# Optimization experiments

Hardware: AMD Instinct MI355X
Metric: run time of the kernel (lower is better)

## Reference

```python
import jax, jax.numpy as jnp
import numpy as np

B, S, DM, DE, H, DH, DC, DCq, DR = 4, 2048, 1024, 1024, 16, 64, 128, 128, 32
SCALE = 1.0 / np.sqrt(DH + DR)


def _rope_tables(seq_len, dim, theta=10000.0):
    inv = 1.0 / (theta ** (jnp.arange(0, dim, 2, dtype=jnp.float32) / dim))  # [dim/2]
    t = jnp.arange(seq_len, dtype=jnp.float32)
    ang = t[:, None] * inv[None, :]  # [S, dim/2]
    return jnp.cos(ang), jnp.sin(ang)


def _apply_rope(xq, xk, cos, sin):
    # xq, xk: [B, S, H, DR]; complex rotary on (even, odd) pairs
    def rot(x):
        s = x.shape
        xr = x.reshape(*s[:-1], s[-1] // 2, 2)
        r, i = xr[..., 0], xr[..., 1]
        c = cos[None, :s[1], None, :]
        sn = sin[None, :s[1], None, :]
        out = jnp.stack([r * c - i * sn, r * sn + i * c], axis=-1)
        return out.reshape(s)
    return rot(xq), rot(xk)


def setup_inputs() -> dict:
    key = jax.random.key(0)
    ks = jax.random.split(key, 10)
    def lin(k, din, dout):
        return 0.02 * jax.random.normal(k, (din, dout), jnp.float32)
    inp = {
        "x": jax.random.normal(ks[0], (B, S, DM), jnp.float32),
        "mask": jnp.tril(jnp.ones((S, S), jnp.float32))[None, None],
        "W_dkv": lin(ks[1], DM, DC),  "b_dkv": jnp.zeros((DC,), jnp.float32),
        "W_dq":  lin(ks[2], DM, DCq), "b_dq":  jnp.zeros((DCq,), jnp.float32),
        "W_uk":  lin(ks[3], DC, DE),  "b_uk":  jnp.zeros((DE,), jnp.float32),
        "W_uv":  lin(ks[4], DC, DE),  "b_uv":  jnp.zeros((DE,), jnp.float32),
        "W_uq":  lin(ks[5], DCq, DE), "b_uq":  jnp.zeros((DE,), jnp.float32),
        "W_qr":  lin(ks[6], DCq, DR * H), "b_qr": jnp.zeros((DR * H,), jnp.float32),
        "W_kr":  lin(ks[7], DM, DR),  "b_kr": jnp.zeros((DR,), jnp.float32),
        "W_o":   lin(ks[8], DE, DM),  "b_o":  jnp.zeros((DM,), jnp.float32),
    }
    return inp


def reference(x, mask, W_dkv, b_dkv, W_dq, b_dq, W_uk, b_uk, W_uv, b_uv,
              W_uq, b_uq, W_qr, b_qr, W_kr, b_kr, W_o, b_o):
    bs, seq_len, _ = x.shape
    cos, sin = _rope_tables(2 * S, DR)

    c_q = x @ W_dq + b_dq            # [B,S,DCq]
    c_kv = x @ W_dkv + b_dkv         # [B,S,DC]
    k_r = x @ W_kr + b_kr            # [B,S,DR]

    q_c = (c_q @ W_uq + b_uq).reshape(bs, seq_len, H, DH)
    k_c = (c_kv @ W_uk + b_uk).reshape(bs, seq_len, H, DH)
    v_c = (c_kv @ W_uv + b_uv).reshape(bs, seq_len, H, DH)

    q_r = (c_q @ W_qr + b_qr).reshape(bs, seq_len, H, DR)
    k_r = jnp.broadcast_to(k_r[:, :, None, :], (bs, seq_len, H, DR))
    q_r, k_r = _apply_rope(q_r, k_r, cos, sin)

    q_t = jnp.concatenate([q_c, q_r], axis=-1)  # [B,S,H,DH+DR]
    k_t = jnp.concatenate([k_c, k_r], axis=-1)

    attn = jnp.einsum('bqhd,bkhd->bhqk', q_t, k_t) * SCALE  # [B,H,S,S]
    m = jnp.where(mask == 0, -jnp.inf, mask)  # faithful masked_fill then add
    attn = attn + m
    p = jax.nn.softmax(attn, axis=-1)
    out = jnp.einsum('bhqk,bkhd->bqhd', p, v_c).reshape(bs, seq_len, H * DH)
    return out @ W_o + b_o
```

## Files before the change

kernel.cpp:

```cpp
#include <hip/hip_runtime.h>
#include <cstdint>
#include <cstddef>

#define S_ 2048
#define B_ 4
#define H_ 16
#define ALPHA_Q 0.14724394f

typedef __attribute__((ext_vector_type(8))) __bf16 bf16x8;
typedef __attribute__((ext_vector_type(4))) __bf16 bf16x4;
typedef __attribute__((ext_vector_type(4))) float f32x4;
typedef __attribute__((ext_vector_type(16))) float f32x16;

__device__ __forceinline__ f32x16 mfma32(bf16x8 a, bf16x8 b, f32x16 c) {
  return __builtin_amdgcn_mfma_f32_32x32x16_bf16(a, b, c, 0, 0, 0);
}

__device__ __forceinline__ void gll16(const void* g, void* l) {
  __builtin_amdgcn_global_load_lds(
      (__attribute__((address_space(1))) void*)(uintptr_t)g,
      (__attribute__((address_space(3))) void*)(uint32_t)(uintptr_t)l,
      16, 0, 0);
}

__device__ __forceinline__ int cvtpk(float lo, float hi) {
  int r;
  asm("v_cvt_pk_bf16_f32 %0, %1, %2" : "=v"(r) : "v"(lo), "v"(hi));
  return r;
}

union PAU { int w[4]; bf16x8 v; };

__device__ __forceinline__ bf16x8 packPA(int hi, float a0, float a1, float a2,
                                         float a3, float b0, float b1, float b2,
                                         float b3) {
  const int Ylo = cvtpk(a0, a1);
  const int Yhi = cvtpk(a2, a3);
  const int Xlo = cvtpk(b0, b1);
  const int Xhi = cvtpk(b2, b3);
  const int t0 = __shfl_xor(hi ? Ylo : Xlo, 32);
  const int t1 = __shfl_xor(hi ? Yhi : Xhi, 32);
  PAU u;
  u.w[0] = hi ? t0 : Ylo;
  u.w[1] = hi ? t1 : Yhi;
  u.w[2] = hi ? Xlo : t0;
  u.w[3] = hi ? Xhi : t1;
  return u.v;
}

__device__ __forceinline__ float tmax16(const f32x16& v) {
  float a[8];
#pragma unroll
  for (int i = 0; i < 8; ++i) a[i] = fmaxf(v[i], v[i + 8]);
#pragma unroll
  for (int s = 4; s > 0; s >>= 1)
#pragma unroll
    for (int i = 0; i < s; ++i) a[i] = fmaxf(a[i], a[i + s]);
  return a[0];
}

__global__ __launch_bounds__(256) void mla_prep(
    const float* __restrict__ x, __bf16* __restrict__ xb,
    const float* __restrict__ W_dq, const float* __restrict__ W_dkv,
    const float* __restrict__ W_kr, const float* __restrict__ W_uq,
    const float* __restrict__ W_qr, const float* __restrict__ W_uk,
    const float* __restrict__ W_uv, const float* __restrict__ W_o,
    __bf16* __restrict__ WdT, __bf16* __restrict__ WuqT,
    __bf16* __restrict__ WukvT, __bf16* __restrict__ WoT,
    const float* __restrict__ b_dq, const float* __restrict__ b_dkv,
    const float* __restrict__ b_kr, const float* __restrict__ b_uq,
    const float* __restrict__ b_qr, const float* __restrict__ b_uk,
    const float* __restrict__ b_uv, float* __restrict__ bias_d,
    float* __restrict__ bias_uq, float* __restrict__ bias_ukv,
    float* __restrict__ ropec, float* __restrict__ ropes) {
  const int id = blockIdx.x;
  const int t = threadIdx.x;
  __shared__ float tile[32][33];

  if (id < 4096) {
    const size_t i = ((size_t)id * 256 + t) * 8;
    float4 a = *(const float4*)&x[i];
    float4 b = *(const float4*)&x[i + 4];
    bf16x8 v;
    v[0] = (__bf16)a.x; v[1] = (__bf16)a.y; v[2] = (__bf16)a.z; v[3] = (__bf16)a.w;
    v[4] = (__bf16)b.x; v[5] = (__bf16)b.y; v[6] = (__bf16)b.z; v[7] = (__bf16)b.w;
    *(bf16x8*)&xb[i] = v;
    return;
  }
  if (id < 5856) {
    int rel = id - 4096;
    const float* W;
    __bf16* WT;
    int K, N, nt;
    if (rel < 128)      { W = W_dq;  WT = WdT;                      K = 1024; N = 128;  nt = 4; }
    else if (rel < 256) { W = W_dkv; WT = WdT + (size_t)128 * 1024; K = 1024; N = 128;  nt = 4;  rel -= 128; }
    else if (rel < 288) { W = W_kr;  WT = WdT + (size_t)256 * 1024; K = 1024; N = 32;   nt = 1;  rel -= 256; }
    else if (rel < 416) { W = W_uq;  WT = WuqT;                     K = 128;  N = 1024; nt = 32; rel -= 288; }
    else if (rel < 480) { W = W_qr;  WT = WuqT + (size_t)1024 * 128; K = 128; N = 512;  nt = 16; rel -= 416; }
    else if (rel < 608) { W = W_uk;  WT = WukvT;                    K = 128;  N = 1024; nt = 32; rel -= 480; }
    else if (rel < 736) { W = W_uv;  WT = WukvT + (size_t)1024 * 128; K = 128; N = 1024; nt = 32; rel -= 608; }
    else                { W = W_o;   WT = WoT;                      K = 1024; N = 1024; nt = 32; rel -= 736; }
    const int n0 = (rel % nt) * 32, k0 = (rel / nt) * 32;
    const int tx = t & 31, ty = t >> 5;
#pragma unroll
    for (int i = 0; i < 32; i += 8)
      tile[ty + i][tx] = W[(size_t)(k0 + ty + i) * N + n0 + tx];
    __syncthreads();
#pragma unroll
    for (int i = 0; i < 32; i += 8)
      WT[(size_t)(n0 + ty + i) * K + k0 + tx] = (__bf16)tile[tx][ty + i];
    return;
  }
  if (id < 5984) {
    const int g = (id - 5856) * 256 + t;
    const int s = g >> 4, i = g & 15;
    const float inv = exp2f(-(float)i * (13.287712379549449f / 16.0f));
    const float ang = (float)s * inv;
    ropec[g] = cosf(ang);
    ropes[g] = sinf(ang);
    return;
  }
  {
    const int g = (id - 5984) * 256 + t;
    if (g < 384)
      bias_d[g] = (g < 128) ? b_dq[g] : (g < 256) ? b_dkv[g - 128]
                 : (g < 288) ? b_kr[g - 256] : 0.f;
    if (g < 1536) bias_uq[g] = (g < 1024) ? b_uq[g] : b_qr[g - 1024];
    if (g < 2048) bias_ukv[g] = (g < 1024) ? b_uk[g] : b_uv[g - 1024];
  }
}

template <int MODE>
__global__ __launch_bounds__(256) void gemm32(
    const __bf16* __restrict__ A, int lda, const __bf16* __restrict__ BT, int ldbt,
    const float* __restrict__ bias, void* __restrict__ C0, int ldc, int K) {
  const int n0 = blockIdx.x * 128;
  const int m0 = blockIdx.y * 128;
  const int wave = threadIdx.x >> 6, lane = threadIdx.x & 63;
  const int hi = lane >> 5, lq = lane & 31;
  const int wm = (wave >> 1) * 64, wn = (wave & 1) * 64;
  __shared__ __bf16 __attribute__((aligned(16))) ldsA[8 * 128 * 8];
  __shared__ __bf16 __attribute__((aligned(16))) ldsB[8 * 128 * 8];

  const f32x16 fz16 = {0.f, 0.f, 0.f, 0.f, 0.f, 0.f, 0.f, 0.f,
                       0.f, 0.f, 0.f, 0.f, 0.f, 0.f, 0.f, 0.f};
  f32x16 acc00 = fz16, acc01 = fz16, acc10 = fz16, acc11 = fz16;

  for (int k0 = 0; k0 < K; k0 += 64) {
    __syncthreads();
#pragma unroll
    for (int i = 0; i < 8; ++i) {
      const int c = wave * 8 + i;
      if (c < 16) {
        const int sl = c >> 1, half = c & 1;
        gll16(&A[(size_t)(m0 + half * 64 + lane) * lda + k0 + sl * 8],
              &ldsA[(sl * 128 + half * 64) * 8]);
      } else {
        const int cc = c - 16;
        const int sl = cc >> 1, half = cc & 1;
        gll16(&BT[(size_t)(n0 + half * 64 + lane) * ldbt + k0 + sl * 8],
              &ldsB[(sl * 128 + half * 64) * 8]);
      }
    }
    __syncthreads();

#pragma unroll
    for (int ks = 0; ks < 4; ++ks) {
      const int sl = ks * 2 + hi;
      bf16x8 a0 = *(const bf16x8*)&ldsA[(sl * 128 + wm + lq) * 8];
      bf16x8 a1 = *(const bf16x8*)&ldsA[(sl * 128 + wm + 32 + lq) * 8];
      bf16x8 b0 = *(const bf16x8*)&ldsB[(sl * 128 + wn + lq) * 8];
      bf16x8 b1 = *(const bf16x8*)&ldsB[(sl * 128 + wn + 32 + lq) * 8];
      acc00 = mfma32(a0, b0, acc00);
      acc01 = mfma32(a0, b1, acc01);
      acc10 = mfma32(a1, b0, acc10);
      acc11 = mfma32(a1, b1, acc11);
    }
  }

  const f32x16* accs[2][2] = {{&acc00, &acc01}, {&acc10, &acc11}};
#pragma unroll
  for (int ni = 0; ni < 2; ++ni) {
    const int col = n0 + wn + ni * 32 + lq;
    const float bv = bias[col];
#pragma unroll
    for (int mi = 0; mi < 2; ++mi) {
      const f32x16& ac = *accs[mi][ni];
#pragma unroll
      for (int r = 0; r < 16; ++r) {
        const int row = m0 + wm + mi * 32 + (r & 3) + 8 * (r >> 2) + 4 * hi;
        const float v = ac[r] + bv;
        if (MODE == 0)
          ((__bf16*)C0)[(size_t)row * ldc + col] = (__bf16)v;
        else
          ((float*)C0)[(size_t)row * ldc + col] = v;
      }
    }
  }
}

__global__ __launch_bounds__(256) void gemm32up(
    const __bf16* __restrict__ cqkvr, const __bf16* __restrict__ WuqT,
    const __bf16* __restrict__ WukvT, const float* __restrict__ bias_uq,
    const float* __restrict__ bias_ukv, __bf16* __restrict__ qt,
    __bf16* __restrict__ qr, __bf16* __restrict__ ktb, __bf16* __restrict__ vv) {
  const bool isQ = blockIdx.x < 12;
  const int n0 = (isQ ? blockIdx.x : (blockIdx.x - 12)) * 128;
  const __bf16* A = cqkvr + (isQ ? 0 : 128);
  const __bf16* BT = isQ ? WuqT : WukvT;
  const float* bias = isQ ? bias_uq : bias_ukv;
  const int m0 = blockIdx.y * 128;
  const int wave = threadIdx.x >> 6, lane = threadIdx.x & 63;
  const int hi = lane >> 5, lq = lane & 31;
  const int wm = (wave >> 1) * 64, wn = (wave & 1) * 64;
  __shared__ __bf16 __attribute__((aligned(16))) ldsA[8 * 128 * 8];
  __shared__ __bf16 __attribute__((aligned(16))) ldsB[8 * 128 * 8];

  const f32x16 fz16 = {0.f, 0.f, 0.f, 0.f, 0.f, 0.f, 0.f, 0.f,
                       0.f, 0.f, 0.f, 0.f, 0.f, 0.f, 0.f, 0.f};
  f32x16 acc00 = fz16, acc01 = fz16, acc10 = fz16, acc11 = fz16;

  for (int k0 = 0; k0 < 128; k0 += 64) {
    __syncthreads();
#pragma unroll
    for (int i = 0; i < 8; ++i) {
      const int c = wave * 8 + i;
      if (c < 16) {
        const int sl = c >> 1, half = c & 1;
        gll16(&A[(size_t)(m0 + half * 64 + lane) * 384 + k0 + sl * 8],
              &ldsA[(sl * 128 + half * 64) * 8]);
      } else {
        const int cc = c - 16;
        const int sl = cc >> 1, half = cc & 1;
        gll16(&BT[(size_t)(n0 + half * 64 + lane) * 128 + k0 + sl * 8],
              &ldsB[(sl * 128 + half * 64) * 8]);
      }
    }
    __syncthreads();

#pragma unroll
    for (int ks = 0; ks < 4; ++ks) {
      const int sl = ks * 2 + hi;
      bf16x8 a0 = *(const bf16x8*)&ldsA[(sl * 128 + wm + lq) * 8];
      bf16x8 a1 = *(const bf16x8*)&ldsA[(sl * 128 + wm + 32 + lq) * 8];
      bf16x8 b0 = *(const bf16x8*)&ldsB[(sl * 128 + wn + lq) * 8];
      bf16x8 b1 = *(const bf16x8*)&ldsB[(sl * 128 + wn + 32 + lq) * 8];
      acc00 = mfma32(a0, b0, acc00);
      acc01 = mfma32(a0, b1, acc01);
      acc10 = mfma32(a1, b0, acc10);
      acc11 = mfma32(a1, b1, acc11);
    }
  }

  const f32x16* accs[2][2] = {{&acc00, &acc01}, {&acc10, &acc11}};
#pragma unroll
  for (int ni = 0; ni < 2; ++ni) {
    const int col = n0 + wn + ni * 32 + lq;
    const float bv = bias[col];
#pragma unroll
    for (int mi = 0; mi < 2; ++mi) {
      const f32x16& ac = *accs[mi][ni];
#pragma unroll
      for (int r = 0; r < 16; ++r) {
        const int row = m0 + wm + mi * 32 + (r & 3) + 8 * (r >> 2) + 4 * hi;
        const float v = ac[r] + bv;
        const int b = row >> 11, s = row & 2047;
        if (col < 1024) {
          const int h = col >> 6, d = col & 63;
          const size_t o = ((size_t)(b * H_ + h) * S_ + s) * 96 + d;
          if (isQ)
            qt[o] = (__bf16)(v * ALPHA_Q);
          else
            ktb[o] = (__bf16)v;
        } else {
          if (isQ)
            qr[(size_t)row * 512 + col - 1024] = (__bf16)v;
          else
            vv[(size_t)row * 1024 + col - 1024] = (__bf16)v;
        }
      }
    }
  }
}

__global__ __launch_bounds__(256) void mla_glue(
    const __bf16* __restrict__ qr, const __bf16* __restrict__ cqkvr,
    const float* __restrict__ ropec, const float* __restrict__ ropes,
    __bf16* __restrict__ qt, __bf16* __restrict__ ktb,
    const __bf16* __restrict__ vv, __bf16* __restrict__ vt) {
  __shared__ __bf16 __attribute__((aligned(16))) tile[64][72];
  const int t = threadIdx.x;
  if (blockIdx.x < 8192) {
    const int gid = blockIdx.x * 256 + t;
    const int bs = gid >> 8;
    const int h = (gid >> 4) & 15;
    const int i = gid & 15;
    const int b = bs >> 11, s = bs & 2047;
    const float c = ropec[s * 16 + i], sn = ropes[s * 16 + i];
    const size_t o = ((size_t)(b * H_ + h) * S_ + s) * 96 + 64 + 2 * i;
    {
      const float r = (float)qr[(size_t)bs * 512 + h * 32 + 2 * i];
      const float im = (float)qr[(size_t)bs * 512 + h * 32 + 2 * i + 1];
      qt[o] = (__bf16)((r * c - im * sn) * ALPHA_Q);
      qt[o + 1] = (__bf16)((r * sn + im * c) * ALPHA_Q);
    }
    {
      const float r = (float)cqkvr[(size_t)bs * 384 + 256 + 2 * i];
      const float im = (float)cqkvr[(size_t)bs * 384 + 256 + 2 * i + 1];
      ktb[o] = (__bf16)(r * c - im * sn);
      ktb[o + 1] = (__bf16)(r * sn + im * c);
    }
    return;
  }
  const int bid = blockIdx.x - 8192;
  const int s0 = (bid & 31) * 64;
  const int bh = bid >> 5;
  const int b = bh >> 4, h = bh & 15;
  {
    const int r = t >> 2, c0 = (t & 3) * 16;
    const size_t src = (size_t)(b * S_ + s0 + r) * 1024 + h * 64 + c0;
    bf16x8 u0 = *(const bf16x8*)&vv[src];
    bf16x8 u1 = *(const bf16x8*)&vv[src + 8];
    *(bf16x8*)&tile[r][c0] = u0;
    *(bf16x8*)&tile[r][c0 + 8] = u1;
  }
  __syncthreads();
  {
    const int d = t >> 2, sc0 = (t & 3) * 16;
    bf16x8 w0, w1;
#pragma unroll
    for (int e = 0; e < 8; ++e) {
      w0[e] = tile[sc0 + e][d];
      w1[e] = tile[sc0 + 8 + e][d];
    }
    const size_t dst = ((size_t)bh * 64 + d) * S_ + s0 + sc0;
    *(bf16x8*)&vt[dst] = w0;
    *(bf16x8*)&vt[dst + 8] = w1;
  }
}

__global__ __launch_bounds__(256, 2) void mla_attn(const __bf16* __restrict__ qt,
                                                   const __bf16* __restrict__ kt,
                                                   const __bf16* __restrict__ vt,
                                                   __bf16* __restrict__ ao) {
  const int bh = blockIdx.x;
  const int j = blockIdx.y;
  const int wave = threadIdx.x >> 6, lane = threadIdx.x & 63;
  const int hi = lane >> 5, lq = lane & 31;
  const __bf16* Q = qt + (size_t)bh * S_ * 96;
  const __bf16* Kp = kt + (size_t)bh * S_ * 96;
  const __bf16* Vp = vt + (size_t)bh * 64 * S_;
  const int bb = bh >> 4, h = bh & 15;

  __shared__ __bf16 __attribute__((aligned(16))) kbuf[2][12 * 512];
  __shared__ __bf16 __attribute__((aligned(16))) vbuf[2][8 * 512];

  const f32x16 fz16 = {0.f, 0.f, 0.f, 0.f, 0.f, 0.f, 0.f, 0.f,
                       0.f, 0.f, 0.f, 0.f, 0.f, 0.f, 0.f, 0.f};
  bf16x8 onesA;
#pragma unroll
  for (int e = 0; e < 8; ++e) onesA[e] = (__bf16)1.0f;

  const int qblkA = j, qblkB = 15 - j;
  const int q0wA = qblkA * 128 + wave * 32;
  const int q0wB = qblkB * 128 + wave * 32;

  bf16x8 qfA[6], qfB[6];
#pragma unroll
  for (int kd = 0; kd < 6; ++kd) {
    qfA[kd] = *(const bf16x8*)&Q[(size_t)(q0wA + lq) * 96 + kd * 16 + hi * 8];
    qfB[kd] = *(const bf16x8*)&Q[(size_t)(q0wB + lq) * 96 + kd * 16 + hi * 8];
  }

  f32x16 o0A = fz16, o1A = fz16, LA = fz16;
  f32x16 o0B = fz16, o1B = fz16, LB = fz16;
  float mA = -3.0e38f, mB = -3.0e38f;

  const int tEndA = (q0wA + 31) >> 6;
  const int tEndB = (q0wB + 31) >> 6;
  const int tMax = qblkB * 2 + 1;

  const __bf16* gsrc[5];
#pragma unroll
  for (int i = 0; i < 5; ++i) {
    const int c = wave + 4 * i;
    gsrc[i] = (c < 12) ? Kp + (size_t)lane * 96 + c * 8
                       : Vp + (size_t)lane * S_ + (c - 12) * 8;
  }
  auto stage = [&](int bsel) {
#pragma unroll
    for (int i = 0; i < 5; ++i) {
      const int c = wave + 4 * i;
      if (c < 12) {
        gll16(gsrc[i], &kbuf[bsel][c * 512]);
        gsrc[i] += 64 * 96;
      } else {
        gll16(gsrc[i], &vbuf[bsel][(c - 12) * 512]);
        gsrc[i] += 64;
      }
    }
  };

  auto process = [&](const bf16x8* qf, f32x16& o0, f32x16& o1, f32x16& Lacc,
                     float& m, int q0w, int tEnd, int t, int bsel) {
    f32x16 s0 = fz16, s1 = fz16;
#pragma unroll
    for (int kd = 0; kd < 6; ++kd) {
      const int sl = kd * 2 + hi;
      bf16x8 a0 = *(const bf16x8*)&kbuf[bsel][(sl * 64 + lq) * 8];
      bf16x8 a1 = *(const bf16x8*)&kbuf[bsel][(sl * 64 + 32 + lq) * 8];
      s0 = mfma32(a0, qf[kd], s0);
      s1 = mfma32(a1, qf[kd], s1);
    }
    if (t == tEnd) {
      const int qg = q0w + lq;
      const int kvb = t * 64 + 4 * hi;
#pragma unroll
      for (int r = 0; r < 16; ++r) {
        const int crow = (r & 3) + 8 * (r >> 2);
        if (kvb + crow > qg) s0[r] = -3.0e38f;
        if (kvb + 32 + crow > qg) s1[r] = -3.0e38f;
      }
    }
    float tm = fmaxf(tmax16(s0), tmax16(s1));
    tm = fmaxf(tm, __shfl_xor(tm, 32));
    if (!__all(tm <= m + 8.0f)) {
      const float mnew = fmaxf(m, tm);
      const float sc = exp2f(m - mnew);
      m = mnew;
      Lacc[0] *= sc;
      o0 *= sc;
      o1 *= sc;
    }
    float p0[16], p1[16];
#pragma unroll
    for (int r = 0; r < 16; ++r) {
      p0[r] = exp2f(s0[r] - m);
      p1[r] = exp2f(s1[r] - m);
    }
    bf16x8 pa[4];
    pa[0] = packPA(hi, p0[0], p0[1], p0[2], p0[3], p0[4], p0[5], p0[6], p0[7]);
    pa[1] = packPA(hi, p0[8], p0[9], p0[10], p0[11], p0[12], p0[13], p0[14], p0[15]);
    pa[2] = packPA(hi, p1[0], p1[1], p1[2], p1[3], p1[4], p1[5], p1[6], p1[7]);
    pa[3] = packPA(hi, p1[8], p1[9], p1[10], p1[11], p1[12], p1[13], p1[14], p1[15]);
#pragma unroll
    for (int ks = 0; ks < 4; ++ks) {
      const int sl = ks * 2 + hi;
      bf16x8 v0 = *(const bf16x8*)&vbuf[bsel][(sl * 64 + lq) * 8];
      bf16x8 v1 = *(const bf16x8*)&vbuf[bsel][(sl * 64 + 32 + lq) * 8];
      o0 = mfma32(v0, pa[ks], o0);
      o1 = mfma32(v1, pa[ks], o1);
      Lacc = mfma32(onesA, pa[ks], Lacc);
    }
  };

  stage(0);
  __syncthreads();

  int bsel = 0;
  for (int t = 0; t <= tMax; ++t) {
    if (t < tMax) stage(bsel ^ 1);
    if (t <= tEndA) process(qfA, o0A, o1A, LA, mA, q0wA, tEndA, t, bsel);
    if (t <= tEndB) process(qfB, o0B, o1B, LB, mB, q0wB, tEndB, t, bsel);
    __syncthreads();
    bsel ^= 1;
  }

  auto writeOut = [&](const f32x16& o0, const f32x16& o1, const f32x16& Lacc,
                      int q0w) {
    const float invL = 1.0f / Lacc[0];
    __bf16* aorow = ao + (size_t)(bb * S_ + q0w + lq) * 1024 + h * 64;
#pragma unroll
    for (int rr = 0; rr < 4; ++rr) {
      bf16x4 w0, w1;
#pragma unroll
      for (int jj = 0; jj < 4; ++jj) {
        w0[jj] = (__bf16)(o0[4 * rr + jj] * invL);
        w1[jj] = (__bf16)(o1[4 * rr + jj] * invL);
      }
      *(bf16x4*)&aorow[rr * 8 + 4 * hi] = w0;
      *(bf16x4*)&aorow[32 + rr * 8 + 4 * hi] = w1;
    }
  };
  writeOut(o0A, o1A, LA, q0wA);
  writeOut(o0B, o1B, LB, q0wB);
}

extern "C" void kernel_launch(void* const* d_in, const int* in_sizes, int n_in,
                              void* d_out, int out_size, void* d_ws, size_t ws_size,
                              hipStream_t stream) {
  (void)in_sizes; (void)n_in; (void)out_size; (void)ws_size;
  const float* x = (const float*)d_in[0];
  const float* W_dkv = (const float*)d_in[2];
  const float* b_dkv = (const float*)d_in[3];
  const float* W_dq = (const float*)d_in[4];
  const float* b_dq = (const float*)d_in[5];
  const float* W_uk = (const float*)d_in[6];
  const float* b_uk = (const float*)d_in[7];
  const float* W_uv = (const float*)d_in[8];
  const float* b_uv = (const float*)d_in[9];
  const float* W_uq = (const float*)d_in[10];
  const float* b_uq = (const float*)d_in[11];
  const float* W_qr = (const float*)d_in[12];
  const float* b_qr = (const float*)d_in[13];
  const float* W_kr = (const float*)d_in[14];
  const float* b_kr = (const float*)d_in[15];
  const float* W_o = (const float*)d_in[16];
  const float* b_o = (const float*)d_in[17];
  float* out = (float*)d_out;

  char* ws = (char*)d_ws;
  size_t off = 0;
  auto take = [&](size_t nbytes) -> char* {
    char* p = ws + off;
    off += (nbytes + 255) & ~(size_t)255;
    return p;
  };
  __bf16* xb = (__bf16*)take((size_t)8192 * 1024 * 2);
  __bf16* WdT = (__bf16*)take((size_t)384 * 1024 * 2);
  __bf16* WuqT = (__bf16*)take((size_t)1536 * 128 * 2);
  __bf16* WukvT = (__bf16*)take((size_t)2048 * 128 * 2);
  __bf16* WoT = (__bf16*)take((size_t)1024 * 1024 * 2);
  float* bias_d = (float*)take(384 * 4);
  float* bias_uq = (float*)take(1536 * 4);
  float* bias_ukv = (float*)take(2048 * 4);
  float* ropec = (float*)take((size_t)S_ * 16 * 4);
  float* ropes = (float*)take((size_t)S_ * 16 * 4);
  __bf16* cqkvr = (__bf16*)take((size_t)8192 * 384 * 2);
  __bf16* qr = (__bf16*)take((size_t)8192 * 512 * 2);
  __bf16* vv = (__bf16*)take((size_t)8192 * 1024 * 2);
  __bf16* qt = (__bf16*)take((size_t)B_ * H_ * S_ * 96 * 2);
  __bf16* ktb = (__bf16*)take((size_t)B_ * H_ * S_ * 96 * 2);
  __bf16* vt = (__bf16*)take((size_t)B_ * H_ * 64 * S_ * 2);
  __bf16* aout = (__bf16*)take((size_t)8192 * 1024 * 2);

  hipMemsetAsync(WdT + (size_t)288 * 1024, 0, (size_t)96 * 1024 * 2, stream);

  mla_prep<<<6000, 256, 0, stream>>>(x, xb, W_dq, W_dkv, W_kr, W_uq, W_qr, W_uk,
                                     W_uv, W_o, WdT, WuqT, WukvT, WoT, b_dq,
                                     b_dkv, b_kr, b_uq, b_qr, b_uk, b_uv, bias_d,
                                     bias_uq, bias_ukv, ropec, ropes);

  gemm32<0><<<dim3(3, 64), 256, 0, stream>>>(xb, 1024, WdT, 1024, bias_d,
                                             cqkvr, 384, 1024);
  gemm32up<<<dim3(28, 64), 256, 0, stream>>>(cqkvr, WuqT, WukvT, bias_uq,
                                             bias_ukv, qt, qr, ktb, vv);

  mla_glue<<<8192 + 2048, 256, 0, stream>>>(qr, cqkvr, ropec, ropes, qt, ktb, vv, vt);

  mla_attn<<<dim3(64, 8), 256, 0, stream>>>(qt, ktb, vt, aout);

  gemm32<1><<<dim3(8, 64), 256, 0, stream>>>(aout, 1024, WoT, 1024, b_o, out,
                                             1024, 1024);
}
```

Measured before the change: 336.6 us.

## Fuse RoPE into GEMM epilogues and share rotary key across heads

RoPE is now applied inside the down- and up-projection GEMM epilogues using lane shuffles, which removes the separate glue pass and the intermediate qr buffer. The rotary key is stored once per batch and position instead of being copied per head, and attention loads it from its own buffer, so K traffic drops. The softmax row sum is now computed with register adds and a shuffle instead of an extra MFMA against a ones vector. The risk is that the epilogues carry more divergent branches and scattered bf16 writes.

```diff
diff --git a/kernel.cpp b/kernel.cpp
--- a/kernel.cpp
+++ b/kernel.cpp
@@ -130,10 +130,11 @@
   }
 }
 
-template <int MODE>
-__global__ __launch_bounds__(256) void gemm32(
-    const __bf16* __restrict__ A, int lda, const __bf16* __restrict__ BT, int ldbt,
-    const float* __restrict__ bias, void* __restrict__ C0, int ldc, int K) {
+__global__ __launch_bounds__(256) void gemm32down(
+    const __bf16* __restrict__ A, const __bf16* __restrict__ BT,
+    const float* __restrict__ bias, const float* __restrict__ ropec,
+    const float* __restrict__ ropes, __bf16* __restrict__ cqkvr,
+    __bf16* __restrict__ krr) {
   const int n0 = blockIdx.x * 128;
   const int m0 = blockIdx.y * 128;
   const int wave = threadIdx.x >> 6, lane = threadIdx.x & 63;
@@ -146,19 +147,19 @@
                        0.f, 0.f, 0.f, 0.f, 0.f, 0.f, 0.f, 0.f};
   f32x16 acc00 = fz16, acc01 = fz16, acc10 = fz16, acc11 = fz16;
 
-  for (int k0 = 0; k0 < K; k0 += 64) {
+  for (int k0 = 0; k0 < 1024; k0 += 64) {
     __syncthreads();
 #pragma unroll
     for (int i = 0; i < 8; ++i) {
       const int c = wave * 8 + i;
       if (c < 16) {
         const int sl = c >> 1, half = c & 1;
-        gll16(&A[(size_t)(m0 + half * 64 + lane) * lda + k0 + sl * 8],
+        gll16(&A[(size_t)(m0 + half * 64 + lane) * 1024 + k0 + sl * 8],
               &ldsA[(sl * 128 + half * 64) * 8]);
       } else {
         const int cc = c - 16;
         const int sl = cc >> 1, half = cc & 1;
-        gll16(&BT[(size_t)(n0 + half * 64 + lane) * ldbt + k0 + sl * 8],
+        gll16(&BT[(size_t)(n0 + half * 64 + lane) * 1024 + k0 + sl * 8],
               &ldsB[(sl * 128 + half * 64) * 8]);
       }
     }
@@ -190,10 +191,17 @@
       for (int r = 0; r < 16; ++r) {
         const int row = m0 + wm + mi * 32 + (r & 3) + 8 * (r >> 2) + 4 * hi;
         const float v = ac[r] + bv;
-        if (MODE == 0)
-          ((__bf16*)C0)[(size_t)row * ldc + col] = (__bf16)v;
-        else
-          ((float*)C0)[(size_t)row * ldc + col] = v;
+        if (col < 256) {
+          cqkvr[(size_t)row * 256 + col] = (__bf16)v;
+        } else if (col < 288) {
+          const int s = row & 2047;
+          const int d = col - 256;
+          const int i2 = d >> 1;
+          const float c = ropec[s * 16 + i2], sn = ropes[s * 16 + i2];
+          const float vp = __shfl_xor(v, 1);
+          const float res = ((d & 1) == 0) ? (v * c - vp * sn) : (vp * sn + v * c);
+          krr[(size_t)row * 32 + d] = (__bf16)res;
+        }
       }
     }
   }
@@ -202,8 +210,9 @@
 __global__ __launch_bounds__(256) void gemm32up(
     const __bf16* __restrict__ cqkvr, const __bf16* __restrict__ WuqT,
     const __bf16* __restrict__ WukvT, const float* __restrict__ bias_uq,
-    const float* __restrict__ bias_ukv, __bf16* __restrict__ qt,
-    __bf16* __restrict__ qr, __bf16* __restrict__ ktb, __bf16* __restrict__ vv) {
+    const float* __restrict__ bias_ukv, const float* __restrict__ ropec,
+    const float* __restrict__ ropes, __bf16* __restrict__ qt,
+    __bf16* __restrict__ ktb, __bf16* __restrict__ vv) {
   const bool isQ = blockIdx.x < 12;
   const int n0 = (isQ ? blockIdx.x : (blockIdx.x - 12)) * 128;
   const __bf16* A = cqkvr + (isQ ? 0 : 128);
@@ -227,7 +236,7 @@
       const int c = wave * 8 + i;
       if (c < 16) {
         const int sl = c >> 1, half = c & 1;
-        gll16(&A[(size_t)(m0 + half * 64 + lane) * 384 + k0 + sl * 8],
+        gll16(&A[(size_t)(m0 + half * 64 + lane) * 256 + k0 + sl * 8],
               &ldsA[(sl * 128 + half * 64) * 8]);
       } else {
         const int cc = c - 16;
@@ -267,54 +276,35 @@
         const int b = row >> 11, s = row & 2047;
         if (col < 1024) {
           const int h = col >> 6, d = col & 63;
-          const size_t o = ((size_t)(b * H_ + h) * S_ + s) * 96 + d;
           if (isQ)
-            qt[o] = (__bf16)(v * ALPHA_Q);
+            qt[((size_t)(b * H_ + h) * S_ + s) * 96 + d] = (__bf16)(v * ALPHA_Q);
           else
-            ktb[o] = (__bf16)v;
+            ktb[((size_t)(b * H_ + h) * S_ + s) * 64 + d] = (__bf16)v;
         } else {
-          if (isQ)
-            qr[(size_t)row * 512 + col - 1024] = (__bf16)v;
-          else
+          if (isQ) {
+            const int dq = col - 1024;
+            const int h = dq >> 5, dd = dq & 31, i2 = dd >> 1;
+            const float c = ropec[s * 16 + i2], sn = ropes[s * 16 + i2];
+            const float vp = __shfl_xor(v, 1);
+            const float res =
+                ((dd & 1) == 0) ? (v * c - vp * sn) : (vp * sn + v * c);
+            qt[((size_t)(b * H_ + h) * S_ + s) * 96 + 64 + dd] =
+                (__bf16)(res * ALPHA_Q);
+          } else {
             vv[(size_t)row * 1024 + col - 1024] = (__bf16)v;
+          }
         }
       }
     }
   }
 }
 
-__global__ __launch_bounds__(256) void mla_glue(
-    const __bf16* __restrict__ qr, const __bf16* __restrict__ cqkvr,
-    const float* __restrict__ ropec, const float* __restrict__ ropes,
-    __bf16* __restrict__ qt, __bf16* __restrict__ ktb,
-    const __bf16* __restrict__ vv, __bf16* __restrict__ vt) {
+__global__ __launch_bounds__(256) void mla_vtrans(const __bf16* __restrict__ vv,
+                                                  __bf16* __restrict__ vt) {
   __shared__ __bf16 __attribute__((aligned(16))) tile[64][72];
   const int t = threadIdx.x;
-  if (blockIdx.x < 8192) {
-    const int gid = blockIdx.x * 256 + t;
-    const int bs = gid >> 8;
-    const int h = (gid >> 4) & 15;
-    const int i = gid & 15;
-    const int b = bs >> 11, s = bs & 2047;
-    const float c = ropec[s * 16 + i], sn = ropes[s * 16 + i];
-    const size_t o = ((size_t)(b * H_ + h) * S_ + s) * 96 + 64 + 2 * i;
-    {
-      const float r = (float)qr[(size_t)bs * 512 + h * 32 + 2 * i];
-      const float im = (float)qr[(size_t)bs * 512 + h * 32 + 2 * i + 1];
-      qt[o] = (__bf16)((r * c - im * sn) * ALPHA_Q);
-      qt[o + 1] = (__bf16)((r * sn + im * c) * ALPHA_Q);
-    }
-    {
-      const float r = (float)cqkvr[(size_t)bs * 384 + 256 + 2 * i];
-      const float im = (float)cqkvr[(size_t)bs * 384 + 256 + 2 * i + 1];
-      ktb[o] = (__bf16)(r * c - im * sn);
-      ktb[o + 1] = (__bf16)(r * sn + im * c);
-    }
-    return;
-  }
-  const int bid = blockIdx.x - 8192;
-  const int s0 = (bid & 31) * 64;
-  const int bh = bid >> 5;
+  const int s0 = (blockIdx.x & 31) * 64;
+  const int bh = blockIdx.x >> 5;
   const int b = bh >> 4, h = bh & 15;
   {
     const int r = t >> 2, c0 = (t & 3) * 16;
@@ -340,26 +330,25 @@
 }
 
 __global__ __launch_bounds__(256, 2) void mla_attn(const __bf16* __restrict__ qt,
-                                                   const __bf16* __restrict__ kt,
+                                                   const __bf16* __restrict__ ktb,
+                                                   const __bf16* __restrict__ krr,
                                                    const __bf16* __restrict__ vt,
                                                    __bf16* __restrict__ ao) {
   const int bh = blockIdx.x;
   const int j = blockIdx.y;
   const int wave = threadIdx.x >> 6, lane = threadIdx.x & 63;
   const int hi = lane >> 5, lq = lane & 31;
+  const int bb = bh >> 4, h = bh & 15;
   const __bf16* Q = qt + (size_t)bh * S_ * 96;
-  const __bf16* Kp = kt + (size_t)bh * S_ * 96;
+  const __bf16* Kp = ktb + (size_t)bh * S_ * 64;
+  const __bf16* Kr = krr + (size_t)bb * S_ * 32;
   const __bf16* Vp = vt + (size_t)bh * 64 * S_;
-  const int bb = bh >> 4, h = bh & 15;
 
   __shared__ __bf16 __attribute__((aligned(16))) kbuf[2][12 * 512];
   __shared__ __bf16 __attribute__((aligned(16))) vbuf[2][8 * 512];
 
   const f32x16 fz16 = {0.f, 0.f, 0.f, 0.f, 0.f, 0.f, 0.f, 0.f,
                        0.f, 0.f, 0.f, 0.f, 0.f, 0.f, 0.f, 0.f};
-  bf16x8 onesA;
-#pragma unroll
-  for (int e = 0; e < 8; ++e) onesA[e] = (__bf16)1.0f;
 
   const int qblkA = j, qblkB = 15 - j;
   const int q0wA = qblkA * 128 + wave * 32;
@@ -372,9 +361,9 @@
     qfB[kd] = *(const bf16x8*)&Q[(size_t)(q0wB + lq) * 96 + kd * 16 + hi * 8];
   }
 
-  f32x16 o0A = fz16, o1A = fz16, LA = fz16;
-  f32x16 o0B = fz16, o1B = fz16, LB = fz16;
-  float mA = -3.0e38f, mB = -3.0e38f;
+  f32x16 o0A = fz16, o1A = fz16;
+  f32x16 o0B = fz16, o1B = fz16;
+  float mA = -3.0e38f, mB = -3.0e38f, LA = 0.f, LB = 0.f;
 
   const int tEndA = (q0wA + 31) >> 6;
   const int tEndB = (q0wB + 31) >> 6;
@@ -384,16 +373,20 @@
 #pragma unroll
   for (int i = 0; i < 5; ++i) {
     const int c = wave + 4 * i;
-    gsrc[i] = (c < 12) ? Kp + (size_t)lane * 96 + c * 8
-                       : Vp + (size_t)lane * S_ + (c - 12) * 8;
+    gsrc[i] = (c < 8)    ? Kp + (size_t)lane * 64 + c * 8
+              : (c < 12) ? Kr + (size_t)lane * 32 + (c - 8) * 8
+                         : Vp + (size_t)lane * S_ + (c - 12) * 8;
   }
   auto stage = [&](int bsel) {
 #pragma unroll
     for (int i = 0; i < 5; ++i) {
       const int c = wave + 4 * i;
-      if (c < 12) {
+      if (c < 8) {
         gll16(gsrc[i], &kbuf[bsel][c * 512]);
-        gsrc[i] += 64 * 96;
+        gsrc[i] += 64 * 64;
+      } else if (c < 12) {
+        gll16(gsrc[i], &kbuf[bsel][c * 512]);
+        gsrc[i] += 64 * 32;
       } else {
         gll16(gsrc[i], &vbuf[bsel][(c - 12) * 512]);
         gsrc[i] += 64;
@@ -401,7 +394,7 @@
     }
   };
 
-  auto process = [&](const bf16x8* qf, f32x16& o0, f32x16& o1, f32x16& Lacc,
+  auto process = [&](const bf16x8* qf, f32x16& o0, f32x16& o1, float& L,
                      float& m, int q0w, int tEnd, int t, int bsel) {
     f32x16 s0 = fz16, s1 = fz16;
 #pragma unroll
@@ -428,7 +421,7 @@
       const float mnew = fmaxf(m, tm);
       const float sc = exp2f(m - mnew);
       m = mnew;
-      Lacc[0] *= sc;
+      L *= sc;
       o0 *= sc;
       o1 *= sc;
     }
@@ -438,6 +431,16 @@
       p0[r] = exp2f(s0[r] - m);
       p1[r] = exp2f(s1[r] - m);
     }
+    float a[16];
+#pragma unroll
+    for (int r = 0; r < 16; ++r) a[r] = p0[r] + p1[r];
+#pragma unroll
+    for (int s = 8; s > 0; s >>= 1)
+#pragma unroll
+      for (int i = 0; i < s; ++i) a[i] += a[i + s];
+    float ps = a[0];
+    ps += __shfl_xor(ps, 32);
+    L += ps;
     bf16x8 pa[4];
     pa[0] = packPA(hi, p0[0], p0[1], p0[2], p0[3], p0[4], p0[5], p0[6], p0[7]);
     pa[1] = packPA(hi, p0[8], p0[9], p0[10], p0[11], p0[12], p0[13], p0[14], p0[15]);
@@ -450,7 +453,6 @@
       bf16x8 v1 = *(const bf16x8*)&vbuf[bsel][(sl * 64 + 32 + lq) * 8];
       o0 = mfma32(v0, pa[ks], o0);
       o1 = mfma32(v1, pa[ks], o1);
-      Lacc = mfma32(onesA, pa[ks], Lacc);
     }
   };
 
@@ -466,9 +468,8 @@
     bsel ^= 1;
   }
 
-  auto writeOut = [&](const f32x16& o0, const f32x16& o1, const f32x16& Lacc,
-                      int q0w) {
-    const float invL = 1.0f / Lacc[0];
+  auto writeOut = [&](const f32x16& o0, const f32x16& o1, float L, int q0w) {
+    const float invL = 1.0f / L;
     __bf16* aorow = ao + (size_t)(bb * S_ + q0w + lq) * 1024 + h * 64;
 #pragma unroll
     for (int rr = 0; rr < 4; ++rr) {
@@ -484,6 +485,70 @@
   };
   writeOut(o0A, o1A, LA, q0wA);
   writeOut(o0B, o1B, LB, q0wB);
+}
+
+__global__ __launch_bounds__(256) void gemm32out(
+    const __bf16* __restrict__ A, const __bf16* __restrict__ BT,
+    const float* __restrict__ bias, float* __restrict__ C) {
+  const int n0 = blockIdx.x * 128;
+  const int m0 = blockIdx.y * 128;
+  const int wave = threadIdx.x >> 6, lane = threadIdx.x & 63;
+  const int hi = lane >> 5, lq = lane & 31;
+  const int wm = (wave >> 1) * 64, wn = (wave & 1) * 64;
+  __shared__ __bf16 __attribute__((aligned(16))) ldsA[8 * 128 * 8];
+  __shared__ __bf16 __attribute__((aligned(16))) ldsB[8 * 128 * 8];
+
+  const f32x16 fz16 = {0.f, 0.f, 0.f, 0.f, 0.f, 0.f, 0.f, 0.f,
+                       0.f, 0.f, 0.f, 0.f, 0.f, 0.f, 0.f, 0.f};
+  f32x16 acc00 = fz16, acc01 = fz16, acc10 = fz16, acc11 = fz16;
+
+  for (int k0 = 0; k0 < 1024; k0 += 64) {
+    __syncthreads();
+#pragma unroll
+    for (int i = 0; i < 8; ++i) {
+      const int c = wave * 8 + i;
+      if (c < 16) {
+        const int sl = c >> 1, half = c & 1;
+        gll16(&A[(size_t)(m0 + half * 64 + lane) * 1024 + k0 + sl * 8],
+              &ldsA[(sl * 128 + half * 64) * 8]);
+      } else {
+        const int cc = c - 16;
+        const int sl = cc >> 1, half = cc & 1;
+        gll16(&BT[(size_t)(n0 + half * 64 + lane) * 1024 + k0 + sl * 8],
+              &ldsB[(sl * 128 + half * 64) * 8]);
+      }
+    }
+    __syncthreads();
+
+#pragma unroll
+    for (int ks = 0; ks < 4; ++ks) {
+      const int sl = ks * 2 + hi;
+      bf16x8 a0 = *(const bf16x8*)&ldsA[(sl * 128 + wm + lq) * 8];
+      bf16x8 a1 = *(const bf16x8*)&ldsA[(sl * 128 + wm + 32 + lq) * 8];
+      bf16x8 b0 = *(const bf16x8*)&ldsB[(sl * 128 + wn + lq) * 8];
+      bf16x8 b1 = *(const bf16x8*)&ldsB[(sl * 128 + wn + 32 + lq) * 8];
+      acc00 = mfma32(a0, b0, acc00);
+      acc01 = mfma32(a0, b1, acc01);
+      acc10 = mfma32(a1, b0, acc10);
+      acc11 = mfma32(a1, b1, acc11);
+    }
+  }
+
+  const f32x16* accs[2][2] = {{&acc00, &acc01}, {&acc10, &acc11}};
+#pragma unroll
+  for (int ni = 0; ni < 2; ++ni) {
+    const int col = n0 + wn + ni * 32 + lq;
+    const float bv = bias[col];
+#pragma unroll
+    for (int mi = 0; mi < 2; ++mi) {
+      const f32x16& ac = *accs[mi][ni];
+#pragma unroll
+      for (int r = 0; r < 16; ++r) {
+        const int row = m0 + wm + mi * 32 + (r & 3) + 8 * (r >> 2) + 4 * hi;
+        C[(size_t)row * 1024 + col] = ac[r] + bv;
+      }
+    }
+  }
 }
 
 extern "C" void kernel_launch(void* const* d_in, const int* in_sizes, int n_in,
@@ -526,30 +591,27 @@
   float* bias_ukv = (float*)take(2048 * 4);
   float* ropec = (float*)take((size_t)S_ * 16 * 4);
   float* ropes = (float*)take((size_t)S_ * 16 * 4);
-  __bf16* cqkvr = (__bf16*)take((size_t)8192 * 384 * 2);
-  __bf16* qr = (__bf16*)take((size_t)8192 * 512 * 2);
+  __bf16* cqkvr = (__bf16*)take((size_t)8192 * 256 * 2);
+  __bf16* krr = (__bf16*)take((size_t)8192 * 32 * 2);
   __bf16* vv = (__bf16*)take((size_t)8192 * 1024 * 2);
   __bf16* qt = (__bf16*)take((size_t)B_ * H_ * S_ * 96 * 2);
-  __bf16* ktb = (__bf16*)take((size_t)B_ * H_ * S_ * 96 * 2);
+  __bf16* ktb = (__bf16*)take((size_t)B_ * H_ * S_ * 64 * 2);
   __bf16* vt = (__bf16*)take((size_t)B_ * H_ * 64 * S_ * 2);
   __bf16* aout = (__bf16*)take((size_t)8192 * 1024 * 2);
-
-  hipMemsetAsync(WdT + (size_t)288 * 1024, 0, (size_t)96 * 1024 * 2, stream);
 
   mla_prep<<<6000, 256, 0, stream>>>(x, xb, W_dq, W_dkv, W_kr, W_uq, W_qr, W_uk,
                                      W_uv, W_o, WdT, WuqT, WukvT, WoT, b_dq,
                                      b_dkv, b_kr, b_uq, b_qr, b_uk, b_uv, bias_d,
                                      bias_uq, bias_ukv, ropec, ropes);
 
-  gemm32<0><<<dim3(3, 64), 256, 0, stream>>>(xb, 1024, WdT, 1024, bias_d,
-                                             cqkvr, 384, 1024);
+  gemm32down<<<dim3(3, 64), 256, 0, stream>>>(xb, WdT, bias_d, ropec, ropes,
+                                              cqkvr, krr);
   gemm32up<<<dim3(28, 64), 256, 0, stream>>>(cqkvr, WuqT, WukvT, bias_uq,
-                                             bias_ukv, qt, qr, ktb, vv);
-
-  mla_glue<<<8192 + 2048, 256, 0, stream>>>(qr, cqkvr, ropec, ropes, qt, ktb, vv, vt);
-
-  mla_attn<<<dim3(64, 8), 256, 0, stream>>>(qt, ktb, vt, aout);
-
-  gemm32<1><<<dim3(8, 64), 256, 0, stream>>>(aout, 1024, WoT, 1024, b_o, out,
-                                             1024, 1024);
-}
+                                             bias_ukv, ropec, ropes, qt, ktb, vv);
+
+  mla_vtrans<<<2048, 256, 0, stream>>>(vv, vt);
+
+  mla_attn<<<dim3(64, 8), 256, 0, stream>>>(qt, ktb, krr, vt, aout);
+
+  gemm32out<<<dim3(8, 64), 256, 0, stream>>>(aout, WoT, b_o, out);
+}
```

New measurement: 355.6 us. 5.6% more time.
